# Kernel tuning notes

Hardware: AMD Instinct MI355X
Metric: run time of the kernel (lower is better)

## Reference

```python
import jax, jax.numpy as jnp
import numpy as np

B, L, D = 2, 1024, 1024
H, KV, CH = 16, 4, 8          # attn heads, kv heads, context-manager heads
HD = D // H                   # 64
E, K, FF = 8, 2, 4 * D        # experts, top-k, ffn hidden
DC = 4                        # conv kernel size
EPS = 1e-6


def setup_inputs() -> dict:
    key = jax.random.key(0)
    ks = jax.random.split(key, 32)
    s = 0.02
    n = lambda k, shp: jax.random.normal(k, shp, jnp.float32) * s
    return {
        'x': jax.random.normal(ks[0], (B, L, D), jnp.float32),
        'mask': jnp.ones((B, L), jnp.int32),
        'w_rms1': jnp.ones((D,), jnp.float32),
        'w_rms2': jnp.ones((D,), jnp.float32),
        'w_rms3': jnp.ones((D,), jnp.float32),
        'w_rms4': jnp.ones((D,), jnp.float32),
        'Wq': n(ks[1], (D, D)), 'Wk': n(ks[2], (D, KV * HD)),
        'Wv': n(ks[3], (D, KV * HD)), 'Wo': n(ks[4], (D, D)),
        'Cq': n(ks[5], (D, D)), 'Ck': n(ks[6], (D, D)),
        'Cv': n(ks[7], (D, D)), 'Co': n(ks[8], (D, D)),
        'Wi': n(ks[9], (D, 2 * D)), 'bi': jnp.zeros((2 * D,), jnp.float32),
        'conv_w': n(ks[10], (D, 1, DC)), 'conv_b': jnp.zeros((D,), jnp.float32),
        'Wod': n(ks[11], (D, D)), 'bod': jnp.zeros((D,), jnp.float32),
        'w_gate': n(ks[12], (E, D)),
        'W1': n(ks[13], (E, D, FF)), 'b1': jnp.zeros((E, FF), jnp.float32),
        'W2': n(ks[14], (E, FF, D)), 'b2': jnp.zeros((E, D), jnp.float32),
    }


def _rmsnorm(x, w):
    rms = jnp.sqrt(jnp.mean(x * x, axis=-1, keepdims=True) + EPS)
    return w * (x / rms)


def _mha(x, mask, Wq, Wk, Wv, Wo, nh, nkv):
    b, l, d = x.shape
    hd = d // nh
    q = (x @ Wq).reshape(b, l, nh, hd)
    k = (x @ Wk).reshape(b, l, nkv, hd)
    v = (x @ Wv).reshape(b, l, nkv, hd)
    if nh != nkv:
        rep = nh // nkv
        k = jnp.repeat(k, rep, axis=2)
        v = jnp.repeat(v, rep, axis=2)
    scores = jnp.einsum('bqhd,bkhd->bhqk', q, k) * (hd ** -0.5)
    scores = jnp.where(mask[:, None, None, :] == 0, -jnp.inf, scores)
    attn = jax.nn.softmax(scores, axis=-1)
    out = jnp.einsum('bhqk,bkhd->bqhd', attn, v).reshape(b, l, d)
    return out @ Wo


def _deltanet(x, Wi, bi, conv_w, conv_b, Wod, bod):
    gv = x @ Wi + bi
    gate, value = jnp.split(gv, 2, axis=-1)
    # depthwise causal conv1d (kernel DC, left pad DC-1, truncated to L)
    v_ncl = jnp.transpose(value, (0, 2, 1))  # [B, D, L]
    conv = jax.lax.conv_general_dilated(
        v_ncl, conv_w, window_strides=(1,), padding=[(DC - 1, 0)],
        feature_group_count=D, dimension_numbers=('NCH', 'OIH', 'NCH'))
    conv = conv + conv_b[None, :, None]
    conv = jnp.transpose(conv, (0, 2, 1))  # [B, L, D]
    gated = conv * jax.nn.silu(gate)
    return gated @ Wod + bod


def _moe(x, w_gate, W1, b1, W2, b2):
    b, l, d = x.shape
    flat = x.reshape(-1, d)                                  # [T, D]
    gate = jax.nn.softmax(flat @ w_gate.T, axis=-1)          # [T, E]
    topk_scores, topk_idx = jax.lax.top_k(gate, K)           # [T, K]
    onehot = jax.nn.one_hot(topk_idx, E, dtype=flat.dtype)   # [T, K, E]
    combine = jnp.sum(topk_scores[..., None] * onehot, axis=1)  # [T, E]
    h = jnp.einsum('td,edh->teh', flat, W1) + b1
    h = jax.nn.gelu(h, approximate=False)
    y = jnp.einsum('teh,ehd->ted', h, W2) + b2
    out = jnp.einsum('ted,te->td', y, combine)
    return out.reshape(b, l, d)


def reference(x, mask, w_rms1, w_rms2, w_rms3, w_rms4,
              Wq, Wk, Wv, Wo, Cq, Ck, Cv, Co,
              Wi, bi, conv_w, conv_b, Wod, bod,
              w_gate, W1, b1, W2, b2):
    # eval mode: dropout = identity. multi_token_pred output is discarded by the block.
    res1 = x
    h = _rmsnorm(x, w_rms1)
    h = res1 + _mha(h, mask, Wq, Wk, Wv, Wo, H, KV)
    res2 = h
    # ContextManager stand-in: 8-head softmax self-attention (source unavailable)
    cm = _mha(h, mask, Cq, Ck, Cv, Co, CH, CH)
    h = res2 + cm
    res3 = h
    g = _rmsnorm(h, w_rms2)
    h = res3 + _deltanet(g, Wi, bi, conv_w, conv_b, Wod, bod)
    res4 = h
    g = _rmsnorm(h, w_rms3)
    h = res4 + _moe(g, w_gate, W1, b1, W2, b2)
    h = _rmsnorm(h, w_rms4)
    return h
```

## Files before the change

### kernel.cpp

```cpp
#include <hip/hip_runtime.h>
#include <hip/hip_bf16.h>
#include <math.h>

#define T_TOK 2048
#define B_SZ 2
#define L_SEQ 1024
#define D_MOD 1024
#define N_H 16
#define N_KV 4
#define N_CH 8
#define N_E 8
#define FF_DIM 4096
#define DC_K 4
#define EPS_F 1e-6f

typedef unsigned short u16;
typedef unsigned int u32;
typedef short s16x8 __attribute__((ext_vector_type(8)));
typedef u16 u16x8 __attribute__((ext_vector_type(8)));
typedef float f32x4 __attribute__((ext_vector_type(4)));
struct alignas(8) U16x4 { u16 a, b, c, d; };

__device__ __forceinline__ float gelu_exact(float x) {
    return 0.5f * x * (1.0f + erff(x * 0.70710678118654752f));
}
__device__ __forceinline__ u16 f2bf(float f) {
    u32 x = __float_as_uint(f);
    return (u16)((x + 0x7fffu + ((x >> 16) & 1u)) >> 16);
}
__device__ __forceinline__ float b2f(u16 u) {
    return __uint_as_float(((u32)u) << 16);
}
__device__ __forceinline__ void gload_lds16(const u16* g, u16* l) {
    __builtin_amdgcn_global_load_lds(
        (const __attribute__((address_space(1))) u32*)g,
        (__attribute__((address_space(3))) u32*)l, 16, 0, 0);
}

__global__ __launch_bounds__(256) void transpose_cvt(const float* __restrict__ src,
                                                     u16* __restrict__ dst,
                                                     int R, int C, int dstStride, int dstRowOff) {
    __shared__ float ts[64][65];
    int e = blockIdx.z;
    src += (size_t)e * R * C;
    dst += (size_t)e * (size_t)C * dstStride;
    int c0 = blockIdx.x * 64, r0 = blockIdx.y * 64;
    int t = threadIdx.x;
#pragma unroll
    for (int k = 0; k < 4; ++k) {
        int fidx = k * 256 + t;
        int r = fidx >> 4, c4 = (fidx & 15) << 2;
        float4 v = *(const float4*)(src + (size_t)(r0 + r) * C + c0 + c4);
        ts[r][c4] = v.x; ts[r][c4 + 1] = v.y; ts[r][c4 + 2] = v.z; ts[r][c4 + 3] = v.w;
    }
    __syncthreads();
#pragma unroll
    for (int k = 0; k < 4; ++k) {
        int idx = k * 256 + t;
        int c = idx >> 4, r4 = (idx & 15) << 2;
        U16x4 o;
        o.a = f2bf(ts[r4][c]);
        o.b = f2bf(ts[r4 + 1][c]);
        o.c = f2bf(ts[r4 + 2][c]);
        o.d = f2bf(ts[r4 + 3][c]);
        *(U16x4*)(dst + (size_t)(dstRowOff + c0 + c) * dstStride + r0 + r4) = o;
    }
}

__global__ __launch_bounds__(256) void rmsnorm_kernel(const float* __restrict__ x,
                                                      const float* __restrict__ w,
                                                      float* __restrict__ fo,
                                                      u16* __restrict__ bo) {
    int row = blockIdx.x;
    int tid = threadIdx.x;
    const float* xr = x + (size_t)row * D_MOD;
    float4 v = ((const float4*)xr)[tid];
    float ss = v.x * v.x + v.y * v.y + v.z * v.z + v.w * v.w;
    __shared__ float red[256];
    red[tid] = ss;
    __syncthreads();
    for (int s = 128; s > 0; s >>= 1) {
        if (tid < s) red[tid] += red[tid + s];
        __syncthreads();
    }
    float inv = 1.0f / sqrtf(red[0] * (1.0f / D_MOD) + EPS_F);
    float4 wv = ((const float4*)w)[tid];
    float4 o;
    o.x = v.x * inv * wv.x;
    o.y = v.y * inv * wv.y;
    o.z = v.z * inv * wv.z;
    o.w = v.w * inv * wv.w;
    if (fo) ((float4*)(fo + (size_t)row * D_MOD))[tid] = o;
    if (bo) {
        U16x4 b;
        b.a = f2bf(o.x); b.b = f2bf(o.y); b.c = f2bf(o.z); b.d = f2bf(o.w);
        *(U16x4*)(bo + (size_t)row * D_MOD + tid * 4) = b;
    }
}

template <int MODE, int GELU, int OUTF, int OUTB, int BM, int BN, int NT>
__global__ __launch_bounds__(NT) void mfma_gemm(const u16* __restrict__ A,
                                                const u16* __restrict__ BT,
                                                const float* __restrict__ bias,
                                                const float* __restrict__ res,
                                                float* __restrict__ C,
                                                u16* __restrict__ Cb,
                                                const int* __restrict__ list,
                                                const int* __restrict__ offs,
                                                const int* __restrict__ counts,
                                                int M, int N, int K, int nx) {
    constexpr int WN = (NT == 512) ? 4 : 2;
    constexpr int PWR = BM / 2;
    constexpr int PWC = BN / WN;
    constexpr int MI = PWR / 16;
    constexpr int NI = PWC / 16;
    constexpr int NAI = (BM * 4) / NT;
    constexpr int NBI = (BN * 4) / NT;
    __shared__ u16 ldsA[2][BM * 32];
    __shared__ u16 ldsB[2][BN * 32];
    int tid = threadIdx.x;
    int lane = tid & 63, w = tid >> 6;
    int wr = w / WN, wc = w % WN;
    int bx, by, e;
    if (MODE == 0) {
        bx = blockIdx.x; by = blockIdx.y; e = 0;
    } else {
        int id = blockIdx.x;
        e = id & 7;
        int r = id >> 3;
        bx = r % nx;
        by = r / nx;
    }
    int cnt, off;
    if (MODE == 0) { cnt = M; off = 0; }
    else { cnt = counts[e]; off = offs[e]; }
    int m0 = by * BM;
    if (m0 >= cnt) return;
    int n0 = bx * BN;
    const u16* Bt = BT + (size_t)e * (size_t)N * K;

    const u16* aSrc[NAI];
    const u16* bSrc[NBI];
#pragma unroll
    for (int j = 0; j < NAI; ++j) {
        int rowA = j * (NT / 4) + w * 16 + (lane >> 2);
        int slot = lane & 3;
        int rl = m0 + rowA;
        if (rl >= cnt) rl = cnt - 1;
        size_t ga;
        if (MODE == 1) ga = (size_t)list[off + rl] * K;
        else if (MODE == 2) ga = (size_t)(off + rl) * K;
        else ga = (size_t)rl * K;
        aSrc[j] = A + ga + ((slot ^ ((rowA >> 1) & 3)) << 3);
    }
#pragma unroll
    for (int j = 0; j < NBI; ++j) {
        int rowB = j * (NT / 4) + w * 16 + (lane >> 2);
        int slot = lane & 3;
        bSrc[j] = Bt + (size_t)(n0 + rowB) * K + ((slot ^ ((rowB >> 1) & 3)) << 3);
    }

    auto stage = [&](int buf, int k0) {
#pragma unroll
        for (int j = 0; j < NAI; ++j)
            gload_lds16(aSrc[j] + k0, &ldsA[buf][(j * NT + w * 64) * 8]);
#pragma unroll
        for (int j = 0; j < NBI; ++j)
            gload_lds16(bSrc[j] + k0, &ldsB[buf][(j * NT + w * 64) * 8]);
    };

    f32x4 acc[MI][NI] = {};
    int r16 = lane & 15, cr = lane >> 4;

    stage(0, 0);
    __syncthreads();
    int cur = 0;
    for (int k0 = 0; k0 < K; k0 += 32) {
        if (k0 + 32 < K) stage(cur ^ 1, k0 + 32);
        s16x8 af[MI], bfr[NI];
#pragma unroll
        for (int mi = 0; mi < MI; ++mi) {
            int row = wr * PWR + mi * 16 + r16;
            af[mi] = *(const s16x8*)&ldsA[cur][row * 32 + ((cr ^ ((row >> 1) & 3)) << 3)];
        }
#pragma unroll
        for (int ni = 0; ni < NI; ++ni) {
            int row = wc * PWC + ni * 16 + r16;
            bfr[ni] = *(const s16x8*)&ldsB[cur][row * 32 + ((cr ^ ((row >> 1) & 3)) << 3)];
        }
#pragma unroll
        for (int mi = 0; mi < MI; ++mi)
#pragma unroll
            for (int ni = 0; ni < NI; ++ni)
                acc[mi][ni] = __builtin_amdgcn_mfma_f32_16x16x32_bf16(af[mi], bfr[ni],
                                                                      acc[mi][ni], 0, 0, 0);
        __syncthreads();
        cur ^= 1;
    }

    const float* bias_e = bias ? (bias + (MODE ? (size_t)e * N : 0)) : nullptr;
#pragma unroll
    for (int mi = 0; mi < MI; ++mi) {
#pragma unroll
        for (int ni = 0; ni < NI; ++ni) {
            int rloc = wr * PWR + mi * 16 + (lane >> 4) * 4;
            int col = n0 + wc * PWC + ni * 16 + (lane & 15);
#pragma unroll
            for (int jj = 0; jj < 4; ++jj) {
                int rl = m0 + rloc + jj;
                if (rl >= cnt) continue;
                float val = acc[mi][ni][jj];
                if (bias_e) val += bias_e[col];
                if (GELU) val = gelu_exact(val);
                size_t crow = (MODE == 0) ? (size_t)rl : (size_t)(off + rl);
                if (res) val += res[crow * N + col];
                if (OUTF) C[crow * N + col] = val;
                if (OUTB) Cb[crow * N + col] = f2bf(val);
            }
        }
    }
}

template <int HD>
__global__ __launch_bounds__(256) void mfma_attn(const u16* __restrict__ Qb,
                                                 const u16* __restrict__ Kb,
                                                 const u16* __restrict__ Vb,
                                                 u16* __restrict__ O,
                                                 int stride, int ostride,
                                                 int nh, int nkv, float scale) {
    constexpr int KT = 64;
    constexpr int CH = HD / 8;
    constexpr int NF = HD / 32;
    constexpr int ND = HD / 16;
    constexpr int VSTR = 72;
    constexpr int NISS = (64 * CH) / (64 * 4);

    __shared__ u16 Kl[64 * HD];
    __shared__ u16 Vt[HD * VSTR];
    __shared__ u16 Pl[4][16 * 72];

    int tid = threadIdx.x, lane = tid & 63, w = tid >> 6;
    int g = lane >> 4, r16 = lane & 15;
    int q0 = blockIdx.x * 64, h = blockIdx.y, b = blockIdx.z;
    int kvh = h / (nh / nkv);

    const u16* Qp = Qb + (size_t)(b * L_SEQ + q0 + w * 16 + r16) * stride + h * HD + g * 8;
    s16x8 qf[NF];
#pragma unroll
    for (int f = 0; f < NF; ++f) qf[f] = *(const s16x8*)(Qp + f * 32);

    const u16* Kbase = Kb + (size_t)(b * L_SEQ) * stride + (size_t)kvh * HD;
    const u16* Vbase = Vb + (size_t)(b * L_SEQ) * stride + (size_t)kvh * HD;

    int srcOffK[NISS];
#pragma unroll
    for (int i = 0; i < NISS; ++i) {
        int ci = (w * NISS + i) * 64 + lane;
        int row = ci / CH;
        int ch = ci % CH;
        srcOffK[i] = row * stride + ((ch ^ (row & 7)) << 3);
    }

    f32x4 ofr[ND] = {};
    float m_r[4], l_r[4];
#pragma unroll
    for (int r = 0; r < 4; ++r) { m_r[r] = -1e30f; l_r[r] = 0.f; }

    for (int kt = 0; kt < L_SEQ / KT; ++kt) {
        const u16* Ksrc = Kbase + (size_t)(kt * KT) * stride;
        const u16* Vsrc = Vbase + (size_t)(kt * KT) * stride;
        __syncthreads();
#pragma unroll
        for (int i = 0; i < NISS; ++i)
            gload_lds16(Ksrc + srcOffK[i], Kl + (size_t)(w * NISS + i) * 512);
#pragma unroll
        for (int half = 0; half < HD / 64; ++half) {
            int dbase = w * 16 + half * 64;
            u16x8 v0 = *(const u16x8*)(Vsrc + (size_t)lane * stride + dbase);
            u16x8 v1 = *(const u16x8*)(Vsrc + (size_t)lane * stride + dbase + 8);
#pragma unroll
            for (int j = 0; j < 8; ++j) {
                Vt[(dbase + j) * VSTR + lane] = v0[j];
                Vt[(dbase + 8 + j) * VSTR + lane] = v1[j];
            }
        }
        __syncthreads();

        f32x4 s[4];
#pragma unroll
        for (int sub = 0; sub < 4; ++sub) {
            f32x4 acc = {};
#pragma unroll
            for (int f = 0; f < NF; ++f) {
                int row = sub * 16 + r16;
                int chunk = (f * 4 + g) ^ (row & 7);
                s16x8 kf = *(const s16x8*)&Kl[(row * CH + chunk) * 8];
                acc = __builtin_amdgcn_mfma_f32_16x16x32_bf16(qf[f], kf, acc, 0, 0, 0);
            }
            s[sub] = acc;
        }

#pragma unroll
        for (int sub = 0; sub < 4; ++sub)
#pragma unroll
            for (int r = 0; r < 4; ++r) s[sub][r] *= scale;
#pragma unroll
        for (int r = 0; r < 4; ++r) {
            float mx = fmaxf(fmaxf(s[0][r], s[1][r]), fmaxf(s[2][r], s[3][r]));
            mx = fmaxf(mx, __shfl_xor(mx, 1));
            mx = fmaxf(mx, __shfl_xor(mx, 2));
            mx = fmaxf(mx, __shfl_xor(mx, 4));
            mx = fmaxf(mx, __shfl_xor(mx, 8));
            float mo = m_r[r];
            float mn = fmaxf(mo, mx);
            float sc = __expf(mo - mn);
            m_r[r] = mn;
            float sum = 0.f;
#pragma unroll
            for (int sub = 0; sub < 4; ++sub) {
                float e = __expf(s[sub][r] - mn);
                s[sub][r] = e;
                sum += e;
            }
            sum += __shfl_xor(sum, 1);
            sum += __shfl_xor(sum, 2);
            sum += __shfl_xor(sum, 4);
            sum += __shfl_xor(sum, 8);
            l_r[r] = l_r[r] * sc + sum;
#pragma unroll
            for (int dsub = 0; dsub < ND; ++dsub) ofr[dsub][r] *= sc;
        }

        u16* Pw = Pl[w];
#pragma unroll
        for (int sub = 0; sub < 4; ++sub)
#pragma unroll
            for (int r = 0; r < 4; ++r) {
                int q = g * 4 + r;
                int k = sub * 16 + r16;
                Pw[q * 72 + (((k >> 3) ^ (q & 7)) << 3) + (k & 7)] = f2bf(s[sub][r]);
            }
        __syncthreads();

        s16x8 pf[2];
#pragma unroll
        for (int ks = 0; ks < 2; ++ks) {
            int chunk = (ks * 4 + g) ^ (r16 & 7);
            pf[ks] = *(const s16x8*)&Pw[r16 * 72 + chunk * 8];
        }
#pragma unroll
        for (int dsub = 0; dsub < ND; ++dsub)
#pragma unroll
            for (int ks = 0; ks < 2; ++ks) {
                s16x8 vf = *(const s16x8*)&Vt[(dsub * 16 + r16) * VSTR + ks * 32 + g * 8];
                ofr[dsub] = __builtin_amdgcn_mfma_f32_16x16x32_bf16(pf[ks], vf, ofr[dsub], 0, 0, 0);
            }
    }

    float inv[4];
#pragma unroll
    for (int r = 0; r < 4; ++r) inv[r] = 1.0f / l_r[r];
#pragma unroll
    for (int dsub = 0; dsub < ND; ++dsub)
#pragma unroll
        for (int r = 0; r < 4; ++r) {
            int q = q0 + w * 16 + g * 4 + r;
            O[(size_t)(b * L_SEQ + q) * ostride + h * HD + dsub * 16 + r16] =
                f2bf(ofr[dsub][r] * inv[r]);
        }
}

__global__ __launch_bounds__(256) void conv_gate_kernel(const u16* __restrict__ gv,
                                                        const float* __restrict__ cw,
                                                        const float* __restrict__ cb,
                                                        u16* __restrict__ gated) {
    int idx = blockIdx.x * 256 + threadIdx.x;
    if (idx >= T_TOK * D_MOD) return;
    int d = idx & (D_MOD - 1);
    int t = idx >> 10;
    int l = t & (L_SEQ - 1);
    float conv = cb[d];
#pragma unroll
    for (int i = 0; i < DC_K; ++i) {
        int lp = l - (DC_K - 1) + i;
        if (lp >= 0)
            conv += b2f(gv[(size_t)(t - l + lp) * (2 * D_MOD) + D_MOD + d]) * cw[d * DC_K + i];
    }
    float gate = b2f(gv[(size_t)t * (2 * D_MOD) + d]);
    float sig = 1.0f / (1.0f + expf(-gate));
    gated[(size_t)t * D_MOD + d] = f2bf(conv * (gate * sig));
}

__global__ __launch_bounds__(256) void route_kernel(const float* __restrict__ g,
                                                    const float* __restrict__ wg,
                                                    int* __restrict__ tIdx,
                                                    float* __restrict__ tScore,
                                                    int* __restrict__ counts) {
    int t = blockIdx.x, tid = threadIdx.x;
    __shared__ float gs[D_MOD];
    __shared__ float logits[N_E];
    ((float4*)gs)[tid] = ((const float4*)(g + (size_t)t * D_MOD))[tid];
    __syncthreads();
    int e = tid >> 5, lane = tid & 31;
    const float* w = wg + (size_t)e * D_MOD;
    float p = 0.f;
    for (int d = lane; d < D_MOD; d += 32) p += gs[d] * w[d];
    for (int o = 16; o > 0; o >>= 1) p += __shfl_down(p, o, 32);
    if (lane == 0) logits[e] = p;
    __syncthreads();
    if (tid == 0) {
        float mx = logits[0];
        for (int e2 = 1; e2 < N_E; ++e2) mx = fmaxf(mx, logits[e2]);
        float pe[N_E];
        float Z = 0.f;
        for (int e2 = 0; e2 < N_E; ++e2) {
            pe[e2] = expf(logits[e2] - mx);
            Z += pe[e2];
        }
        int i0 = 0;
        float b0 = pe[0];
        for (int e2 = 1; e2 < N_E; ++e2)
            if (pe[e2] > b0) { b0 = pe[e2]; i0 = e2; }
        int i1 = -1;
        float b1 = -1.f;
        for (int e2 = 0; e2 < N_E; ++e2)
            if (e2 != i0 && pe[e2] > b1) { b1 = pe[e2]; i1 = e2; }
        float invZ = 1.0f / Z;
        tIdx[t * 2] = i0;
        tIdx[t * 2 + 1] = i1;
        tScore[t * 2] = b0 * invZ;
        tScore[t * 2 + 1] = b1 * invZ;
        atomicAdd(&counts[i0], 1);
        atomicAdd(&counts[i1], 1);
    }
}

__global__ void prefix_kernel(const int* __restrict__ counts, int* __restrict__ offs,
                              int* __restrict__ cursor) {
    if (threadIdx.x == 0) {
        int acc = 0;
        for (int e = 0; e < N_E; ++e) {
            offs[e] = acc;
            acc += counts[e];
            cursor[e] = 0;
        }
    }
}

__global__ __launch_bounds__(256) void fill_kernel(const int* __restrict__ tIdx,
                                                   const int* __restrict__ offs,
                                                   int* __restrict__ cursor,
                                                   int* __restrict__ list,
                                                   int* __restrict__ pairRow) {
    int t = blockIdx.x * 256 + threadIdx.x;
    if (t >= T_TOK) return;
    for (int kk = 0; kk < 2; ++kk) {
        int e = tIdx[t * 2 + kk];
        int pos = atomicAdd(&cursor[e], 1);
        int slot = offs[e] + pos;
        list[slot] = t;
        pairRow[t * 2 + kk] = slot;
    }
}

__global__ __launch_bounds__(256) void combine_kernel(const u16* __restrict__ ysel,
                                                      const float* __restrict__ tScore,
                                                      const int* __restrict__ pairRow,
                                                      float* __restrict__ h) {
    int idx = blockIdx.x * 256 + threadIdx.x;
    if (idx >= T_TOK * D_MOD) return;
    int t = idx >> 10;
    int d = idx & (D_MOD - 1);
    float acc = h[idx];
#pragma unroll
    for (int kk = 0; kk < 2; ++kk) {
        int r = pairRow[t * 2 + kk];
        acc += tScore[t * 2 + kk] * b2f(ysel[(size_t)r * D_MOD + d]);
    }
    h[idx] = acc;
}

extern "C" void kernel_launch(void* const* d_in, const int* in_sizes, int n_in,
                              void* d_out, int out_size, void* d_ws, size_t ws_size,
                              hipStream_t stream) {
    const float* x = (const float*)d_in[0];
    const float* w_rms1 = (const float*)d_in[2];
    const float* w_rms2 = (const float*)d_in[3];
    const float* w_rms3 = (const float*)d_in[4];
    const float* w_rms4 = (const float*)d_in[5];
    const float* Wq = (const float*)d_in[6];
    const float* Wk = (const float*)d_in[7];
    const float* Wv = (const float*)d_in[8];
    const float* Wo = (const float*)d_in[9];
    const float* Cq = (const float*)d_in[10];
    const float* Ck = (const float*)d_in[11];
    const float* Cv = (const float*)d_in[12];
    const float* Co = (const float*)d_in[13];
    const float* Wi = (const float*)d_in[14];
    const float* bi = (const float*)d_in[15];
    const float* conv_w = (const float*)d_in[16];
    const float* conv_b = (const float*)d_in[17];
    const float* Wod = (const float*)d_in[18];
    const float* bod = (const float*)d_in[19];
    const float* w_gate = (const float*)d_in[20];
    const float* W1 = (const float*)d_in[21];
    const float* b1 = (const float*)d_in[22];
    const float* W2 = (const float*)d_in[23];
    const float* b2 = (const float*)d_in[24];
    float* out = (float*)d_out;

    char* ws = (char*)d_ws;
    size_t off = 0;
    auto alloc_f = [&](size_t n) { float* p = (float*)(ws + off); off += n * 4; return p; };
    auto alloc_b = [&](size_t n) { u16* p = (u16*)(ws + off); off += n * 2; return p; };

    u16* qkvT = alloc_b((size_t)1536 * 1024);
    u16* cqkvT = alloc_b((size_t)3072 * 1024);
    u16* WoT = alloc_b((size_t)1024 * 1024);
    u16* CoT = alloc_b((size_t)1024 * 1024);
    u16* WiT = alloc_b((size_t)2048 * 1024);
    u16* WodT = alloc_b((size_t)1024 * 1024);
    u16* W1T = alloc_b((size_t)N_E * FF_DIM * 1024);
    u16* W2T = alloc_b((size_t)N_E * 1024 * FF_DIM);
    const size_t TD = (size_t)T_TOK * D_MOD;
    float* h = alloc_f(TD);
    float* nrm = alloc_f(TD);
    u16* nrm_bf = alloc_b(TD);
    u16* h_bf = alloc_b(TD);
    u16* ab_bf = alloc_b(TD);
    u16* qkv_bf = alloc_b((size_t)T_TOK * 3072);
    u16* gv_bf = alloc_b((size_t)T_TOK * 2048);
    u16* hsel = alloc_b((size_t)2 * T_TOK * FF_DIM);
    u16* ysel = alloc_b((size_t)2 * T_TOK * D_MOD);
    int* counts = (int*)(ws + off); off += N_E * 4;
    int* offs = (int*)(ws + off); off += N_E * 4;
    int* cursor = (int*)(ws + off); off += N_E * 4;
    int* tIdx = (int*)(ws + off); off += 2 * T_TOK * 4;
    int* list = (int*)(ws + off); off += 2 * T_TOK * 4;
    int* pairRow = (int*)(ws + off); off += 2 * T_TOK * 4;
    float* tScore = alloc_f(2 * T_TOK);

    transpose_cvt<<<dim3(16, 16, 1), 256, 0, stream>>>(Wq, qkvT, 1024, 1024, 1024, 0);
    transpose_cvt<<<dim3(4, 16, 1), 256, 0, stream>>>(Wk, qkvT, 1024, 256, 1024, 1024);
    transpose_cvt<<<dim3(4, 16, 1), 256, 0, stream>>>(Wv, qkvT, 1024, 256, 1024, 1280);
    transpose_cvt<<<dim3(16, 16, 1), 256, 0, stream>>>(Cq, cqkvT, 1024, 1024, 1024, 0);
    transpose_cvt<<<dim3(16, 16, 1), 256, 0, stream>>>(Ck, cqkvT, 1024, 1024, 1024, 1024);
    transpose_cvt<<<dim3(16, 16, 1), 256, 0, stream>>>(Cv, cqkvT, 1024, 1024, 1024, 2048);
    transpose_cvt<<<dim3(16, 16, 1), 256, 0, stream>>>(Wo, WoT, 1024, 1024, 1024, 0);
    transpose_cvt<<<dim3(16, 16, 1), 256, 0, stream>>>(Co, CoT, 1024, 1024, 1024, 0);
    transpose_cvt<<<dim3(32, 16, 1), 256, 0, stream>>>(Wi, WiT, 1024, 2048, 1024, 0);
    transpose_cvt<<<dim3(16, 16, 1), 256, 0, stream>>>(Wod, WodT, 1024, 1024, 1024, 0);
    transpose_cvt<<<dim3(64, 16, N_E), 256, 0, stream>>>(W1, W1T, 1024, FF_DIM, 1024, 0);
    transpose_cvt<<<dim3(16, 64, N_E), 256, 0, stream>>>(W2, W2T, FF_DIM, 1024, FF_DIM, 0);

    rmsnorm_kernel<<<T_TOK, 256, 0, stream>>>(x, w_rms1, nullptr, nrm_bf);
    mfma_gemm<0, 0, 0, 1, 64, 128, 256><<<dim3(12, 32, 1), 256, 0, stream>>>(
        nrm_bf, qkvT, nullptr, nullptr, nullptr, qkv_bf, nullptr, nullptr, nullptr,
        T_TOK, 1536, 1024, 0);
    mfma_attn<64><<<dim3(16, N_H, B_SZ), 256, 0, stream>>>(
        qkv_bf, qkv_bf + 1024, qkv_bf + 1280, ab_bf, 1536, 1024, N_H, N_KV, 0.125f);
    mfma_gemm<0, 0, 1, 1, 64, 128, 256><<<dim3(8, 32, 1), 256, 0, stream>>>(
        ab_bf, WoT, nullptr, x, h, h_bf, nullptr, nullptr, nullptr, T_TOK, 1024, 1024, 0);

    mfma_gemm<0, 0, 0, 1, 64, 128, 256><<<dim3(24, 32, 1), 256, 0, stream>>>(
        h_bf, cqkvT, nullptr, nullptr, nullptr, qkv_bf, nullptr, nullptr, nullptr,
        T_TOK, 3072, 1024, 0);
    mfma_attn<128><<<dim3(16, N_CH, B_SZ), 256, 0, stream>>>(
        qkv_bf, qkv_bf + 1024, qkv_bf + 2048, ab_bf, 3072, 1024, N_CH, N_CH,
        0.088388347648318447f);
    mfma_gemm<0, 0, 1, 0, 64, 128, 256><<<dim3(8, 32, 1), 256, 0, stream>>>(
        ab_bf, CoT, nullptr, h, h, nullptr, nullptr, nullptr, nullptr, T_TOK, 1024, 1024, 0);

    rmsnorm_kernel<<<T_TOK, 256, 0, stream>>>(h, w_rms2, nullptr, nrm_bf);
    mfma_gemm<0, 0, 0, 1, 64, 128, 256><<<dim3(16, 32, 1), 256, 0, stream>>>(
        nrm_bf, WiT, bi, nullptr, nullptr, gv_bf, nullptr, nullptr, nullptr, T_TOK, 2048, 1024, 0);
    conv_gate_kernel<<<(T_TOK * D_MOD) / 256, 256, 0, stream>>>(gv_bf, conv_w, conv_b, ab_bf);
    mfma_gemm<0, 0, 1, 0, 64, 128, 256><<<dim3(8, 32, 1), 256, 0, stream>>>(
        ab_bf, WodT, bod, h, h, nullptr, nullptr, nullptr, nullptr, T_TOK, 1024, 1024, 0);

    rmsnorm_kernel<<<T_TOK, 256, 0, stream>>>(h, w_rms3, nrm, nrm_bf);
    hipMemsetAsync(counts, 0, N_E * sizeof(int), stream);
    route_kernel<<<T_TOK, 256, 0, stream>>>(nrm, w_gate, tIdx, tScore, counts);
    prefix_kernel<<<1, 64, 0, stream>>>(counts, offs, cursor);
    fill_kernel<<<(T_TOK + 255) / 256, 256, 0, stream>>>(tIdx, offs, cursor, list, pairRow);
    mfma_gemm<1, 1, 0, 1, 128, 128, 256><<<32 * 16 * 8, 256, 0, stream>>>(
        nrm_bf, W1T, b1, nullptr, nullptr, hsel, list, offs, counts, T_TOK, FF_DIM, 1024, 32);
    mfma_gemm<2, 0, 0, 1, 64, 128, 256><<<8 * 32 * 8, 256, 0, stream>>>(
        hsel, W2T, b2, nullptr, nullptr, ysel, list, offs, counts, T_TOK, 1024, FF_DIM, 8);
    combine_kernel<<<(T_TOK * D_MOD) / 256, 256, 0, stream>>>(ysel, tScore, pairRow, h);

    rmsnorm_kernel<<<T_TOK, 256, 0, stream>>>(h, w_rms4, out, nullptr);
}
```

Measured before the change: 674.7 us.

## Batch weight transposes into one launch, fuse combine+final RMSNorm, shrink W2 tile

Replaces twelve transpose launches with a single descriptor-driven kernel covering all weight matrices, which removes launch overhead and tail gaps. Merges the MoE combine step with the final RMSNorm into one per-row kernel, so the extra read and write of h goes away. The GEMM template now fixes BN=128 and supports BM=32, which the W2 expert GEMM uses to launch more blocks for better load balance across uneven expert counts, at the cost of less A-tile reuse.

```diff
diff --git a/kernel.cpp b/kernel.cpp
--- a/kernel.cpp
+++ b/kernel.cpp
@@ -37,33 +37,48 @@
         (__attribute__((address_space(3))) u32*)l, 16, 0, 0);
 }
 
-__global__ __launch_bounds__(256) void transpose_cvt(const float* __restrict__ src,
-                                                     u16* __restrict__ dst,
-                                                     int R, int C, int dstStride, int dstRowOff) {
+struct TDesc {
+    const float* src;
+    u16* dst;
+    int R, C, dstStride, dstRowOff, tileBase, nPerMat;
+};
+struct TPack { TDesc d[12]; };
+
+__global__ __launch_bounds__(256) void transpose_all(TPack p) {
     __shared__ float ts[64][65];
-    int e = blockIdx.z;
-    src += (size_t)e * R * C;
-    dst += (size_t)e * (size_t)C * dstStride;
-    int c0 = blockIdx.x * 64, r0 = blockIdx.y * 64;
-    int t = threadIdx.x;
+    int t = blockIdx.x;
+    int i = 0;
+#pragma unroll
+    for (int j = 1; j < 12; ++j)
+        if (t >= p.d[j].tileBase) i = j;
+    TDesc d = p.d[i];
+    int local = t - d.tileBase;
+    int e = local / d.nPerMat;
+    local -= e * d.nPerMat;
+    int ntx = d.C >> 6;
+    int bx = local % ntx, by = local / ntx;
+    const float* src = d.src + (size_t)e * d.R * d.C;
+    u16* dst = d.dst + (size_t)e * (size_t)d.C * d.dstStride;
+    int c0 = bx * 64, r0 = by * 64;
+    int tid = threadIdx.x;
 #pragma unroll
     for (int k = 0; k < 4; ++k) {
-        int fidx = k * 256 + t;
+        int fidx = k * 256 + tid;
         int r = fidx >> 4, c4 = (fidx & 15) << 2;
-        float4 v = *(const float4*)(src + (size_t)(r0 + r) * C + c0 + c4);
+        float4 v = *(const float4*)(src + (size_t)(r0 + r) * d.C + c0 + c4);
         ts[r][c4] = v.x; ts[r][c4 + 1] = v.y; ts[r][c4 + 2] = v.z; ts[r][c4 + 3] = v.w;
     }
     __syncthreads();
 #pragma unroll
     for (int k = 0; k < 4; ++k) {
-        int idx = k * 256 + t;
+        int idx = k * 256 + tid;
         int c = idx >> 4, r4 = (idx & 15) << 2;
         U16x4 o;
         o.a = f2bf(ts[r4][c]);
         o.b = f2bf(ts[r4 + 1][c]);
         o.c = f2bf(ts[r4 + 2][c]);
         o.d = f2bf(ts[r4 + 3][c]);
-        *(U16x4*)(dst + (size_t)(dstRowOff + c0 + c) * dstStride + r0 + r4) = o;
+        *(U16x4*)(dst + (size_t)(d.dstRowOff + c0 + c) * d.dstStride + r0 + r4) = o;
     }
 }
 
@@ -98,29 +113,26 @@
     }
 }
 
-template <int MODE, int GELU, int OUTF, int OUTB, int BM, int BN, int NT>
-__global__ __launch_bounds__(NT) void mfma_gemm(const u16* __restrict__ A,
-                                                const u16* __restrict__ BT,
-                                                const float* __restrict__ bias,
-                                                const float* __restrict__ res,
-                                                float* __restrict__ C,
-                                                u16* __restrict__ Cb,
-                                                const int* __restrict__ list,
-                                                const int* __restrict__ offs,
-                                                const int* __restrict__ counts,
-                                                int M, int N, int K, int nx) {
-    constexpr int WN = (NT == 512) ? 4 : 2;
+template <int MODE, int GELU, int OUTF, int OUTB, int BM>
+__global__ __launch_bounds__(256) void mfma_gemm(const u16* __restrict__ A,
+                                                 const u16* __restrict__ BT,
+                                                 const float* __restrict__ bias,
+                                                 const float* __restrict__ res,
+                                                 float* __restrict__ C,
+                                                 u16* __restrict__ Cb,
+                                                 const int* __restrict__ list,
+                                                 const int* __restrict__ offs,
+                                                 const int* __restrict__ counts,
+                                                 int M, int N, int K, int nx) {
     constexpr int PWR = BM / 2;
-    constexpr int PWC = BN / WN;
     constexpr int MI = PWR / 16;
-    constexpr int NI = PWC / 16;
-    constexpr int NAI = (BM * 4) / NT;
-    constexpr int NBI = (BN * 4) / NT;
+    constexpr int NI = 4;
+    constexpr int NAI = (BM >= 64) ? (BM / 64) : 1;
     __shared__ u16 ldsA[2][BM * 32];
-    __shared__ u16 ldsB[2][BN * 32];
+    __shared__ u16 ldsB[2][128 * 32];
     int tid = threadIdx.x;
     int lane = tid & 63, w = tid >> 6;
-    int wr = w / WN, wc = w % WN;
+    int wr = w >> 1, wc = w & 1;
     int bx, by, e;
     if (MODE == 0) {
         bx = blockIdx.x; by = blockIdx.y; e = 0;
@@ -136,16 +148,18 @@
     else { cnt = counts[e]; off = offs[e]; }
     int m0 = by * BM;
     if (m0 >= cnt) return;
-    int n0 = bx * BN;
+    int n0 = bx * 128;
     const u16* Bt = BT + (size_t)e * (size_t)N * K;
 
     const u16* aSrc[NAI];
-    const u16* bSrc[NBI];
+    const u16* bSrc[2];
 #pragma unroll
     for (int j = 0; j < NAI; ++j) {
-        int rowA = j * (NT / 4) + w * 16 + (lane >> 2);
+        int rowA = (BM >= 64) ? (j * 64 + w * 16 + (lane >> 2))
+                              : ((w & 1) * 16 + (lane >> 2));
+        if (BM == 32) rowA = w * 16 + (lane >> 2);
         int slot = lane & 3;
-        int rl = m0 + rowA;
+        int rl = m0 + ((rowA < BM) ? rowA : (BM - 1));
         if (rl >= cnt) rl = cnt - 1;
         size_t ga;
         if (MODE == 1) ga = (size_t)list[off + rl] * K;
@@ -154,19 +168,23 @@
         aSrc[j] = A + ga + ((slot ^ ((rowA >> 1) & 3)) << 3);
     }
 #pragma unroll
-    for (int j = 0; j < NBI; ++j) {
-        int rowB = j * (NT / 4) + w * 16 + (lane >> 2);
+    for (int j = 0; j < 2; ++j) {
+        int rowB = j * 64 + w * 16 + (lane >> 2);
         int slot = lane & 3;
         bSrc[j] = Bt + (size_t)(n0 + rowB) * K + ((slot ^ ((rowB >> 1) & 3)) << 3);
     }
 
     auto stage = [&](int buf, int k0) {
-#pragma unroll
-        for (int j = 0; j < NAI; ++j)
-            gload_lds16(aSrc[j] + k0, &ldsA[buf][(j * NT + w * 64) * 8]);
-#pragma unroll
-        for (int j = 0; j < NBI; ++j)
-            gload_lds16(bSrc[j] + k0, &ldsB[buf][(j * NT + w * 64) * 8]);
+        if constexpr (BM == 32) {
+            if (w < 2) gload_lds16(aSrc[0] + k0, &ldsA[buf][w * 512]);
+        } else {
+#pragma unroll
+            for (int j = 0; j < NAI; ++j)
+                gload_lds16(aSrc[j] + k0, &ldsA[buf][(j * 256 + w * 64) * 8]);
+        }
+#pragma unroll
+        for (int j = 0; j < 2; ++j)
+            gload_lds16(bSrc[j] + k0, &ldsB[buf][(j * 256 + w * 64) * 8]);
     };
 
     f32x4 acc[MI][NI] = {};
@@ -185,7 +203,7 @@
         }
 #pragma unroll
         for (int ni = 0; ni < NI; ++ni) {
-            int row = wc * PWC + ni * 16 + r16;
+            int row = wc * 64 + ni * 16 + r16;
             bfr[ni] = *(const s16x8*)&ldsB[cur][row * 32 + ((cr ^ ((row >> 1) & 3)) << 3)];
         }
 #pragma unroll
@@ -204,7 +222,7 @@
 #pragma unroll
         for (int ni = 0; ni < NI; ++ni) {
             int rloc = wr * PWR + mi * 16 + (lane >> 4) * 4;
-            int col = n0 + wc * PWC + ni * 16 + (lane & 15);
+            int col = n0 + wc * 64 + ni * 16 + (lane & 15);
 #pragma unroll
             for (int jj = 0; jj < 4; ++jj) {
                 int rl = m0 + rloc + jj;
@@ -463,21 +481,38 @@
     }
 }
 
-__global__ __launch_bounds__(256) void combine_kernel(const u16* __restrict__ ysel,
-                                                      const float* __restrict__ tScore,
-                                                      const int* __restrict__ pairRow,
-                                                      float* __restrict__ h) {
-    int idx = blockIdx.x * 256 + threadIdx.x;
-    if (idx >= T_TOK * D_MOD) return;
-    int t = idx >> 10;
-    int d = idx & (D_MOD - 1);
-    float acc = h[idx];
-#pragma unroll
-    for (int kk = 0; kk < 2; ++kk) {
-        int r = pairRow[t * 2 + kk];
-        acc += tScore[t * 2 + kk] * b2f(ysel[(size_t)r * D_MOD + d]);
-    }
-    h[idx] = acc;
+__global__ __launch_bounds__(256) void combine_rms_kernel(const u16* __restrict__ ysel,
+                                                          const float* __restrict__ tScore,
+                                                          const int* __restrict__ pairRow,
+                                                          const float* __restrict__ h,
+                                                          const float* __restrict__ w,
+                                                          float* __restrict__ out) {
+    int row = blockIdx.x;
+    int tid = threadIdx.x;
+    float4 v = ((const float4*)(h + (size_t)row * D_MOD))[tid];
+    int r0 = pairRow[row * 2], r1 = pairRow[row * 2 + 1];
+    float s0 = tScore[row * 2], s1 = tScore[row * 2 + 1];
+    U16x4 y0 = *(const U16x4*)(ysel + (size_t)r0 * D_MOD + tid * 4);
+    U16x4 y1 = *(const U16x4*)(ysel + (size_t)r1 * D_MOD + tid * 4);
+    v.x += s0 * b2f(y0.a) + s1 * b2f(y1.a);
+    v.y += s0 * b2f(y0.b) + s1 * b2f(y1.b);
+    v.z += s0 * b2f(y0.c) + s1 * b2f(y1.c);
+    v.w += s0 * b2f(y0.d) + s1 * b2f(y1.d);
+    __shared__ float red[256];
+    red[tid] = v.x * v.x + v.y * v.y + v.z * v.z + v.w * v.w;
+    __syncthreads();
+    for (int s = 128; s > 0; s >>= 1) {
+        if (tid < s) red[tid] += red[tid + s];
+        __syncthreads();
+    }
+    float inv = 1.0f / sqrtf(red[0] * (1.0f / D_MOD) + EPS_F);
+    float4 wv = ((const float4*)w)[tid];
+    float4 o;
+    o.x = v.x * inv * wv.x;
+    o.y = v.y * inv * wv.y;
+    o.z = v.z * inv * wv.z;
+    o.w = v.w * inv * wv.w;
+    ((float4*)(out + (size_t)row * D_MOD))[tid] = o;
 }
 
 extern "C" void kernel_launch(void* const* d_in, const int* in_sizes, int n_in,
@@ -540,42 +575,50 @@
     int* pairRow = (int*)(ws + off); off += 2 * T_TOK * 4;
     float* tScore = alloc_f(2 * T_TOK);
 
-    transpose_cvt<<<dim3(16, 16, 1), 256, 0, stream>>>(Wq, qkvT, 1024, 1024, 1024, 0);
-    transpose_cvt<<<dim3(4, 16, 1), 256, 0, stream>>>(Wk, qkvT, 1024, 256, 1024, 1024);
-    transpose_cvt<<<dim3(4, 16, 1), 256, 0, stream>>>(Wv, qkvT, 1024, 256, 1024, 1280);
-    transpose_cvt<<<dim3(16, 16, 1), 256, 0, stream>>>(Cq, cqkvT, 1024, 1024, 1024, 0);
-    transpose_cvt<<<dim3(16, 16, 1), 256, 0, stream>>>(Ck, cqkvT, 1024, 1024, 1024, 1024);
-    transpose_cvt<<<dim3(16, 16, 1), 256, 0, stream>>>(Cv, cqkvT, 1024, 1024, 1024, 2048);
-    transpose_cvt<<<dim3(16, 16, 1), 256, 0, stream>>>(Wo, WoT, 1024, 1024, 1024, 0);
-    transpose_cvt<<<dim3(16, 16, 1), 256, 0, stream>>>(Co, CoT, 1024, 1024, 1024, 0);
-    transpose_cvt<<<dim3(32, 16, 1), 256, 0, stream>>>(Wi, WiT, 1024, 2048, 1024, 0);
-    transpose_cvt<<<dim3(16, 16, 1), 256, 0, stream>>>(Wod, WodT, 1024, 1024, 1024, 0);
-    transpose_cvt<<<dim3(64, 16, N_E), 256, 0, stream>>>(W1, W1T, 1024, FF_DIM, 1024, 0);
-    transpose_cvt<<<dim3(16, 64, N_E), 256, 0, stream>>>(W2, W2T, FF_DIM, 1024, FF_DIM, 0);
+    TPack tp;
+    int tb = 0;
+    auto mkd = [&](int i, const float* s, u16* d, int R, int C, int ds, int ro, int nmat) {
+        int per = (C >> 6) * (R >> 6);
+        tp.d[i] = TDesc{s, d, R, C, ds, ro, tb, per};
+        tb += per * nmat;
+    };
+    mkd(0, Wq, qkvT, 1024, 1024, 1024, 0, 1);
+    mkd(1, Wk, qkvT, 1024, 256, 1024, 1024, 1);
+    mkd(2, Wv, qkvT, 1024, 256, 1024, 1280, 1);
+    mkd(3, Cq, cqkvT, 1024, 1024, 1024, 0, 1);
+    mkd(4, Ck, cqkvT, 1024, 1024, 1024, 1024, 1);
+    mkd(5, Cv, cqkvT, 1024, 1024, 1024, 2048, 1);
+    mkd(6, Wo, WoT, 1024, 1024, 1024, 0, 1);
+    mkd(7, Co, CoT, 1024, 1024, 1024, 0, 1);
+    mkd(8, Wi, WiT, 1024, 2048, 1024, 0, 1);
+    mkd(9, Wod, WodT, 1024, 1024, 1024, 0, 1);
+    mkd(10, W1, W1T, 1024, FF_DIM, 1024, 0, N_E);
+    mkd(11, W2, W2T, FF_DIM, 1024, FF_DIM, 0, N_E);
+    transpose_all<<<tb, 256, 0, stream>>>(tp);
 
     rmsnorm_kernel<<<T_TOK, 256, 0, stream>>>(x, w_rms1, nullptr, nrm_bf);
-    mfma_gemm<0, 0, 0, 1, 64, 128, 256><<<dim3(12, 32, 1), 256, 0, stream>>>(
+    mfma_gemm<0, 0, 0, 1, 64><<<dim3(12, 32, 1), 256, 0, stream>>>(
         nrm_bf, qkvT, nullptr, nullptr, nullptr, qkv_bf, nullptr, nullptr, nullptr,
         T_TOK, 1536, 1024, 0);
     mfma_attn<64><<<dim3(16, N_H, B_SZ), 256, 0, stream>>>(
         qkv_bf, qkv_bf + 1024, qkv_bf + 1280, ab_bf, 1536, 1024, N_H, N_KV, 0.125f);
-    mfma_gemm<0, 0, 1, 1, 64, 128, 256><<<dim3(8, 32, 1), 256, 0, stream>>>(
+    mfma_gemm<0, 0, 1, 1, 64><<<dim3(8, 32, 1), 256, 0, stream>>>(
         ab_bf, WoT, nullptr, x, h, h_bf, nullptr, nullptr, nullptr, T_TOK, 1024, 1024, 0);
 
-    mfma_gemm<0, 0, 0, 1, 64, 128, 256><<<dim3(24, 32, 1), 256, 0, stream>>>(
+    mfma_gemm<0, 0, 0, 1, 64><<<dim3(24, 32, 1), 256, 0, stream>>>(
         h_bf, cqkvT, nullptr, nullptr, nullptr, qkv_bf, nullptr, nullptr, nullptr,
         T_TOK, 3072, 1024, 0);
     mfma_attn<128><<<dim3(16, N_CH, B_SZ), 256, 0, stream>>>(
         qkv_bf, qkv_bf + 1024, qkv_bf + 2048, ab_bf, 3072, 1024, N_CH, N_CH,
         0.088388347648318447f);
-    mfma_gemm<0, 0, 1, 0, 64, 128, 256><<<dim3(8, 32, 1), 256, 0, stream>>>(
+    mfma_gemm<0, 0, 1, 0, 64><<<dim3(8, 32, 1), 256, 0, stream>>>(
         ab_bf, CoT, nullptr, h, h, nullptr, nullptr, nullptr, nullptr, T_TOK, 1024, 1024, 0);
 
     rmsnorm_kernel<<<T_TOK, 256, 0, stream>>>(h, w_rms2, nullptr, nrm_bf);
-    mfma_gemm<0, 0, 0, 1, 64, 128, 256><<<dim3(16, 32, 1), 256, 0, stream>>>(
+    mfma_gemm<0, 0, 0, 1, 64><<<dim3(16, 32, 1), 256, 0, stream>>>(
         nrm_bf, WiT, bi, nullptr, nullptr, gv_bf, nullptr, nullptr, nullptr, T_TOK, 2048, 1024, 0);
     conv_gate_kernel<<<(T_TOK * D_MOD) / 256, 256, 0, stream>>>(gv_bf, conv_w, conv_b, ab_bf);
-    mfma_gemm<0, 0, 1, 0, 64, 128, 256><<<dim3(8, 32, 1), 256, 0, stream>>>(
+    mfma_gemm<0, 0, 1, 0, 64><<<dim3(8, 32, 1), 256, 0, stream>>>(
         ab_bf, WodT, bod, h, h, nullptr, nullptr, nullptr, nullptr, T_TOK, 1024, 1024, 0);
 
     rmsnorm_kernel<<<T_TOK, 256, 0, stream>>>(h, w_rms3, nrm, nrm_bf);
@@ -583,11 +626,9 @@
     route_kernel<<<T_TOK, 256, 0, stream>>>(nrm, w_gate, tIdx, tScore, counts);
     prefix_kernel<<<1, 64, 0, stream>>>(counts, offs, cursor);
     fill_kernel<<<(T_TOK + 255) / 256, 256, 0, stream>>>(tIdx, offs, cursor, list, pairRow);
-    mfma_gemm<1, 1, 0, 1, 128, 128, 256><<<32 * 16 * 8, 256, 0, stream>>>(
+    mfma_gemm<1, 1, 0, 1, 128><<<32 * 16 * 8, 256, 0, stream>>>(
         nrm_bf, W1T, b1, nullptr, nullptr, hsel, list, offs, counts, T_TOK, FF_DIM, 1024, 32);
-    mfma_gemm<2, 0, 0, 1, 64, 128, 256><<<8 * 32 * 8, 256, 0, stream>>>(
+    mfma_gemm<2, 0, 0, 1, 32><<<8 * 64 * 8, 256, 0, stream>>>(
         hsel, W2T, b2, nullptr, nullptr, ysel, list, offs, counts, T_TOK, 1024, FF_DIM, 8);
-    combine_kernel<<<(T_TOK * D_MOD) / 256, 256, 0, stream>>>(ysel, tScore, pairRow, h);
-
-    rmsnorm_kernel<<<T_TOK, 256, 0, stream>>>(h, w_rms4, out, nullptr);
-}
+    combine_rms_kernel<<<T_TOK, 256, 0, stream>>>(ysel, tScore, pairRow, h, w_rms4, out);
+}
```

Measured after the change: 644.6 us. -4.5%, faster.
